# Optimization experiments

Hardware: AMD Instinct MI355X
Metric: run time of the kernel (lower is better)

## Reference

```python
import jax, jax.numpy as jnp
import numpy as np

D, H, KVH, HD = 2048, 16, 8, 128
D1, D2 = 32, 64  # get_decompose_dim(2048)
BITS = 8


def fake_quant(x, bits=BITS):
    # per-row (last-axis) symmetric fake quant with straight-through estimator
    qmax = float(2 ** (bits - 1) - 1)
    s = jnp.maximum(jnp.max(jnp.abs(x), axis=-1, keepdims=True) / qmax, 1e-8)
    q = jnp.clip(jnp.round(x / s), -qmax, qmax) * s
    return x + jax.lax.stop_gradient(q - x)


def rotate_half(x):
    h = x.shape[-1] // 2
    return jnp.concatenate([-x[..., h:], x[..., :h]], axis=-1)


def setup_inputs() -> dict:
    key = jax.random.key(0)
    ks = jax.random.split(key, 10)
    B, S = 1, 2048
    hidden_states = jax.random.normal(ks[0], (B, S, D), jnp.float32)
    # rotary embeddings
    inv_freq = 1.0 / (10000.0 ** (jnp.arange(0, HD, 2, dtype=jnp.float32) / HD))
    t = jnp.arange(S, dtype=jnp.float32)
    freqs = t[:, None] * inv_freq[None, :]
    emb = jnp.concatenate([freqs, freqs], axis=-1)
    cos, sin = jnp.cos(emb)[None], jnp.sin(emb)[None]  # [1,S,HD]
    # projection weights
    Wq = jax.random.normal(ks[1], (H * HD, D), jnp.float32) * 0.02
    Wk = jax.random.normal(ks[2], (KVH * HD, D), jnp.float32) * 0.02
    Wv = jax.random.normal(ks[3], (KVH * HD, D), jnp.float32) * 0.02
    Wo = jax.random.normal(ks[4], (D, H * HD), jnp.float32) * 0.02
    # learned invertible transforms (near-identity for conditioning)
    L = jnp.eye(D1) + 0.02 * jax.random.normal(ks[5], (D1, D1), jnp.float32)
    R = jnp.eye(D2) + 0.02 * jax.random.normal(ks[6], (D2, D2), jnp.float32)
    diag = 1.0 + 0.1 * jax.random.uniform(ks[7], (D,), jnp.float32)
    Tk = jnp.eye(HD) + 0.02 * jax.random.normal(ks[8], (HD, HD), jnp.float32)
    Tv = jnp.eye(HD) + 0.02 * jax.random.normal(ks[9], (HD, HD), jnp.float32)
    return dict(hidden_states=hidden_states, cos=cos, sin=sin, Wq=Wq, Wk=Wk,
                Wv=Wv, Wo=Wo, L=L, R=R, diag=diag, Tk=Tk, Tv=Tv)


def reference(hidden_states, cos, sin, Wq, Wk, Wv, Wo, L, R, diag, Tk, Tv):
    B, S, _ = hidden_states.shape
    groups = H // KVH
    scale = HD ** -0.5
    # ---- ln_trans: x' = (x * diag) @ kron(L, R) ----
    P = diag[:, None] * jnp.kron(L, R)               # [D, D]
    Pinv = jnp.kron(jnp.linalg.inv(L), jnp.linalg.inv(R)) * (1.0 / diag)[None, :]
    x = hidden_states @ P
    x_q = fake_quant(x)                               # per-token activation quant
    # ---- QKV with transform fused into weights (qa_trans), then weight quant ----
    q = x_q @ fake_quant(Wq @ Pinv.T).T               # [B,S,H*HD]
    k = x_q @ fake_quant(Wk @ Pinv.T).T               # [B,S,KVH*HD]
    Wv_eff = jnp.einsum('hd,khD->kdD', Tv, (Wv @ Pinv.T).reshape(KVH, HD, D))
    v = x_q @ fake_quant(Wv_eff.reshape(KVH * HD, D)).T  # v already in Tv space
    # ---- heads + RoPE ----
    q = q.reshape(B, S, H, HD).transpose(0, 2, 1, 3)
    k = k.reshape(B, S, KVH, HD).transpose(0, 2, 1, 3)
    v = v.reshape(B, S, KVH, HD).transpose(0, 2, 1, 3)
    c, s_ = cos[:, None], sin[:, None]                # [1,1,S,HD]
    q = q * c + rotate_half(q) * s_
    k = k * c + rotate_half(k) * s_
    # ---- kcache trans + quant: q @ inv(Tk)^T, k @ Tk (dot product preserved) ----
    q = q @ jnp.linalg.inv(Tk).T
    k = fake_quant(k @ Tk)
    v = fake_quant(v)
    # ---- eager causal attention with GQA ----
    k = jnp.repeat(k, groups, axis=1)
    v = jnp.repeat(v, groups, axis=1)
    scores = jnp.einsum('bhqd,bhkd->bhqk', q, k) * scale
    mask = jnp.tril(jnp.ones((S, S), bool))
    scores = jnp.where(mask, scores, jnp.finfo(scores.dtype).min)
    w = jax.nn.softmax(scores, axis=-1)
    o = jnp.einsum('bhqk,bhkd->bhqd', w, v)
    o = o.transpose(0, 2, 1, 3).reshape(B, S, H * HD)
    # ---- undo vcache trans per head, then quantized o_proj ----
    o = (o.reshape(B, S, H, HD) @ jnp.linalg.inv(Tv)).reshape(B, S, H * HD)
    out = fake_quant(o) @ fake_quant(Wo).T
    return out
```

## Files before the change

kernel.cpp:

```cpp
#include <hip/hip_runtime.h>
#include <math.h>

typedef unsigned short u16;
typedef __attribute__((ext_vector_type(8))) short bf16x8;
typedef __attribute__((ext_vector_type(4))) float f32x4;

__device__ __forceinline__ u16 f2bf(float x) {
    union { float f; unsigned int u; } c; c.f = x;
    unsigned int r = c.u + 0x7fffu + ((c.u >> 16) & 1u);
    return (u16)(r >> 16);
}
__device__ __forceinline__ float bf2f(u16 h) {
    union { unsigned int u; float f; } c; c.u = ((unsigned int)h) << 16;
    return c.f;
}
__device__ __forceinline__ bf16x8 ld16(const u16* p) {
    bf16x8 r;
    ((uint2*)&r)[0] = *(const uint2*)p;
    ((uint2*)&r)[1] = *(const uint2*)(p + 4);
    return r;
}
__device__ __forceinline__ void st8(u16* dst, uint4 r) {
    *(uint2*)dst = make_uint2(r.x, r.y);
    *(uint2*)(dst + 4) = make_uint2(r.z, r.w);
}
__device__ __forceinline__ void cvt8(const float4& v0, const float4& v1,
                                     uint4& hi, uint4& lo) {
    float vv[8] = {v0.x, v0.y, v0.z, v0.w, v1.x, v1.y, v1.z, v1.w};
    u16 h[8], l[8];
#pragma unroll
    for (int e = 0; e < 8; ++e) {
        h[e] = f2bf(vv[e]);
        l[e] = f2bf(vv[e] - bf2f(h[e]));
    }
    hi.x = h[0] | ((unsigned)h[1] << 16); hi.y = h[2] | ((unsigned)h[3] << 16);
    hi.z = h[4] | ((unsigned)h[5] << 16); hi.w = h[6] | ((unsigned)h[7] << 16);
    lo.x = l[0] | ((unsigned)l[1] << 16); lo.y = l[2] | ((unsigned)l[3] << 16);
    lo.z = l[4] | ((unsigned)l[5] << 16); lo.w = l[6] | ((unsigned)l[7] << 16);
}

__global__ __launch_bounds__(1024) void gj4_kernel(
    const float* __restrict__ A0, float* __restrict__ I0,
    const float* __restrict__ A1, float* __restrict__ I1,
    const float* __restrict__ A2, float* __restrict__ I2,
    const float* __restrict__ A3, float* __restrict__ I3) {
    __shared__ float rowbuf[2][128];
    const float* A; float* out; int N;
    switch (blockIdx.x) {
        case 0:  A = A0; out = I0; N = 32;  break;
        case 1:  A = A1; out = I1; N = 64;  break;
        case 2:  A = A2; out = I2; N = 128; break;
        default: A = A3; out = I3; N = 128; break;
    }
    const int tid = threadIdx.x;
    const int i = tid >> 3, g = tid & 7, c0 = g * 16;
    const int rl = (i & 7) << 3;
    float r[16];
#pragma unroll
    for (int e = 0; e < 16; ++e) {
        int j = c0 + e;
        r[e] = (i < N && j < N) ? A[i * N + j] : ((i == j) ? 1.0f : 0.0f);
    }
    if (i == 0) {
        float ip = 1.0f / __shfl(r[0], rl, 64);
#pragma unroll
        for (int e = 0; e < 16; ++e)
            rowbuf[0][c0 + e] = (c0 + e == 0) ? ip : r[e] * ip;
    }
    __syncthreads();
    const int ng = N >> 4;
    for (int k16 = 0; k16 < ng; ++k16) {
#pragma unroll
        for (int e = 0; e < 16; ++e) {
            const int k = (k16 << 4) + e;
            const int pb = k & 1;
            float ci = __shfl(r[e], rl + k16, 64);
            float4 rb0 = *(const float4*)&rowbuf[pb][c0];
            float4 rb1 = *(const float4*)&rowbuf[pb][c0 + 4];
            float4 rb2 = *(const float4*)&rowbuf[pb][c0 + 8];
            float4 rb3 = *(const float4*)&rowbuf[pb][c0 + 12];
            float rb[16] = {rb0.x, rb0.y, rb0.z, rb0.w, rb1.x, rb1.y, rb1.z, rb1.w,
                            rb2.x, rb2.y, rb2.z, rb2.w, rb3.x, rb3.y, rb3.z, rb3.w};
            if (i == k) {
#pragma unroll
                for (int e2 = 0; e2 < 16; ++e2) r[e2] = rb[e2];
            } else {
#pragma unroll
                for (int e2 = 0; e2 < 16; ++e2) {
                    float v = (c0 + e2 == k) ? 0.0f : r[e2];
                    r[e2] = fmaf(-ci, rb[e2], v);
                }
            }
            if (k + 1 < N && i == k + 1) {
                const int en = (e + 1) & 15;
                const int gn = (e == 15) ? k16 + 1 : k16;
                float ip = 1.0f / __shfl(r[en], rl + gn, 64);
#pragma unroll
                for (int e2 = 0; e2 < 16; ++e2)
                    rowbuf[pb ^ 1][c0 + e2] = (c0 + e2 == k + 1) ? ip : r[e2] * ip;
            }
            __syncthreads();
        }
    }
    if (i < N)
#pragma unroll
        for (int e = 0; e < 16; ++e) {
            int j = c0 + e;
            if (j < N) out[i * N + j] = r[e];
        }
}

template <int TA, int TB, int OUTQ, int DIV>
__global__ __launch_bounds__(256) void kron_kernel(
    const float* __restrict__ X, const float* __restrict__ scIn,
    const float* __restrict__ A, const float* __restrict__ B,
    u16* __restrict__ Yq, float* __restrict__ Ysc, float* __restrict__ Yf) {
    __shared__ float Al[32 * 33];
    __shared__ float Bl[64 * 65];
    __shared__ float Xl[32 * 65];
    __shared__ float Tl[32 * 65];
    __shared__ float red[256];
    const int tid = threadIdx.x;
    for (int idx = tid; idx < 1024; idx += 256) {
        int c = idx >> 5, a = idx & 31;
        Al[c * 33 + a] = TA ? A[a * 32 + c] : A[c * 32 + a];
    }
    for (int idx = tid; idx < 4096; idx += 256) {
        int d = idx >> 6, b = idx & 63;
        Bl[d * 65 + b] = TB ? B[b * 64 + d] : B[d * 64 + b];
    }
    const int row = blockIdx.x;
    const float* xp = X + (size_t)row * 2048;
    for (int j = tid; j < 2048; j += 256) {
        float sc = DIV ? (1.0f / scIn[j]) : scIn[j];
        Xl[(j >> 6) * 65 + (j & 63)] = xp[j] * sc;
    }
    __syncthreads();

    const int c = tid >> 3, b0 = (tid & 7) * 8;
    float t[8];
#pragma unroll
    for (int jj = 0; jj < 8; ++jj) t[jj] = 0.0f;
    for (int d = 0; d < 64; ++d) {
        float xv = Xl[c * 65 + d];
#pragma unroll
        for (int jj = 0; jj < 8; ++jj)
            t[jj] = fmaf(xv, Bl[d * 65 + b0 + jj], t[jj]);
    }
#pragma unroll
    for (int jj = 0; jj < 8; ++jj) Tl[c * 65 + b0 + jj] = t[jj];
    __syncthreads();

    const int a = tid >> 3;
    float y[8];
#pragma unroll
    for (int jj = 0; jj < 8; ++jj) y[jj] = 0.0f;
    for (int c2 = 0; c2 < 32; ++c2) {
        float av = Al[c2 * 33 + a];
#pragma unroll
        for (int jj = 0; jj < 8; ++jj)
            y[jj] = fmaf(av, Tl[c2 * 65 + b0 + jj], y[jj]);
    }

    if (OUTQ) {
        float am = 0.0f;
#pragma unroll
        for (int jj = 0; jj < 8; ++jj) am = fmaxf(am, fabsf(y[jj]));
        red[tid] = am;
        __syncthreads();
        for (int s = 128; s > 0; s >>= 1) {
            if (tid < s) red[tid] = fmaxf(red[tid], red[tid + s]);
            __syncthreads();
        }
        float scale = fmaxf(red[0] / 127.0f, 1e-8f);
        if (tid == 0) Ysc[row] = scale;
        u16 qq[8];
#pragma unroll
        for (int e = 0; e < 8; ++e) {
            float v = rintf(y[e] / scale);
            v = fminf(fmaxf(v, -127.0f), 127.0f);
            qq[e] = f2bf(v);
        }
        uint4 pk;
        pk.x = qq[0] | ((unsigned)qq[1] << 16); pk.y = qq[2] | ((unsigned)qq[3] << 16);
        pk.z = qq[4] | ((unsigned)qq[5] << 16); pk.w = qq[6] | ((unsigned)qq[7] << 16);
        *(uint4*)(Yq + (size_t)row * 2048 + tid * 8) = pk;
    } else {
        float* yp = Yf + (size_t)row * 2048 + tid * 8;
        *(float4*)yp = make_float4(y[0], y[1], y[2], y[3]);
        *(float4*)(yp + 4) = make_float4(y[4], y[5], y[6], y[7]);
    }
}

__global__ void split_s_kernel(const float* __restrict__ in, int ld, int cols,
                               u16* __restrict__ hi, u16* __restrict__ lo) {
    int idx = (blockIdx.x * 256 + threadIdx.x) * 4;
    int r = idx / cols, c = idx % cols;
    float4 v = *(const float4*)(in + (size_t)r * ld + c);
    ushort4 h, l;
    h.x = f2bf(v.x); l.x = f2bf(v.x - bf2f(h.x));
    h.y = f2bf(v.y); l.y = f2bf(v.y - bf2f(h.y));
    h.z = f2bf(v.z); l.z = f2bf(v.z - bf2f(h.z));
    h.w = f2bf(v.w); l.w = f2bf(v.w - bf2f(h.w));
    *(ushort4*)(hi + idx) = h;
    *(ushort4*)(lo + idx) = l;
}

__global__ void split_t_kernel(const float* __restrict__ in, u16* __restrict__ hi,
                               u16* __restrict__ lo, int rows, int cols) {
    __shared__ float t[32][33];
    int bx = blockIdx.x, by = blockIdx.y;
    int lx = threadIdx.x & 31, ly = threadIdx.x >> 5;
    for (int r = ly; r < 32; r += 8)
        t[r][lx] = in[(size_t)(by * 32 + r) * cols + bx * 32 + lx];
    __syncthreads();
    for (int r = ly; r < 32; r += 8) {
        float v = t[lx][r];
        size_t o = (size_t)(bx * 32 + r) * rows + by * 32 + lx;
        u16 h = f2bf(v);
        hi[o] = h;
        lo[o] = f2bf(v - bf2f(h));
    }
}

__global__ void split_t3_kernel(const float* __restrict__ i0, u16* __restrict__ h0,
                                u16* __restrict__ l0,
                                const float* __restrict__ i1, u16* __restrict__ h1,
                                u16* __restrict__ l1,
                                const float* __restrict__ i2, u16* __restrict__ h2,
                                u16* __restrict__ l2) {
    __shared__ float t[32][33];
    const float* in; u16* hi; u16* lo;
    switch (blockIdx.z) {
        case 0:  in = i0; hi = h0; lo = l0; break;
        case 1:  in = i1; hi = h1; lo = l1; break;
        default: in = i2; hi = h2; lo = l2; break;
    }
    int bx = blockIdx.x, by = blockIdx.y;
    int lx = threadIdx.x & 31, ly = threadIdx.x >> 5;
    for (int r = ly; r < 32; r += 8)
        t[r][lx] = in[(size_t)(by * 32 + r) * 128 + bx * 32 + lx];
    __syncthreads();
    for (int r = ly; r < 32; r += 8) {
        float v = t[lx][r];
        size_t o = (size_t)(bx * 32 + r) * 128 + by * 32 + lx;
        u16 h = f2bf(v);
        hi[o] = h;
        lo[o] = f2bf(v - bf2f(h));
    }
}

__global__ __launch_bounds__(256) void gemm_kernel(
    const u16* __restrict__ Ah, const u16* __restrict__ Al, int lda, long aZ, int aDiv,
    const u16* __restrict__ Bh, const u16* __restrict__ Bl, int ldb, long bZ, int bDiv,
    float* __restrict__ C, int ldc, long cZ, int cDiv, int K, float alpha) {
    const int m0 = blockIdx.y * 128, n0 = blockIdx.x * 128;
    const int z = blockIdx.z;
    {
        long ao = (long)(z >> aDiv) * aZ;
        long bo = (long)(z >> bDiv) * bZ;
        Ah += ao; Al += ao; Bh += bo; Bl += bo;
    }
    __shared__ u16 Ash[2][2][128][36];
    __shared__ u16 Bsh[2][2][128][36];

    const int tid = threadIdx.x, lane = tid & 63, wave = tid >> 6;
    const int wr = wave >> 1, wc = wave & 1;
    const int fr = lane & 15, fg8 = (lane >> 4) * 8;
    const int srow = tid >> 2, cc8 = (tid & 3) * 8;

    f32x4 acc[4][4];
#pragma unroll
    for (int m = 0; m < 4; ++m)
#pragma unroll
        for (int n = 0; n < 4; ++n) acc[m][n] = (f32x4)0.0f;

    uint4 rah0, rah1, ral0, ral1, rbh0, rbh1, rbl0, rbl1;
    const size_t aoff0 = (size_t)(m0 + srow) * lda + cc8;
    const size_t aoff1 = aoff0 + (size_t)64 * lda;
    const size_t boff0 = (size_t)(n0 + srow) * ldb + cc8;
    const size_t boff1 = boff0 + (size_t)64 * ldb;

#define G_LOAD(k0) { \
    rah0 = *(const uint4*)(Ah + aoff0 + (k0)); rah1 = *(const uint4*)(Ah + aoff1 + (k0)); \
    ral0 = *(const uint4*)(Al + aoff0 + (k0)); ral1 = *(const uint4*)(Al + aoff1 + (k0)); \
    rbh0 = *(const uint4*)(Bh + boff0 + (k0)); rbh1 = *(const uint4*)(Bh + boff1 + (k0)); \
    rbl0 = *(const uint4*)(Bl + boff0 + (k0)); rbl1 = *(const uint4*)(Bl + boff1 + (k0)); }
#define G_STORE(b) { \
    st8(&Ash[b][0][srow][cc8], rah0); st8(&Ash[b][0][srow + 64][cc8], rah1); \
    st8(&Ash[b][1][srow][cc8], ral0); st8(&Ash[b][1][srow + 64][cc8], ral1); \
    st8(&Bsh[b][0][srow][cc8], rbh0); st8(&Bsh[b][0][srow + 64][cc8], rbh1); \
    st8(&Bsh[b][1][srow][cc8], rbl0); st8(&Bsh[b][1][srow + 64][cc8], rbl1); }

    const int nk = K >> 5;
    G_LOAD(0);
    G_STORE(0);
    __syncthreads();
    int cur = 0;
    for (int ik = 0; ik < nk; ++ik) {
        if (ik + 1 < nk) G_LOAD((ik + 1) << 5);
        bf16x8 bh[4], bl[4];
#pragma unroll
        for (int n = 0; n < 4; ++n) {
            bh[n] = ld16(&Bsh[cur][0][wc * 64 + n * 16 + fr][fg8]);
            bl[n] = ld16(&Bsh[cur][1][wc * 64 + n * 16 + fr][fg8]);
        }
#pragma unroll
        for (int m = 0; m < 4; ++m) {
            bf16x8 ah = ld16(&Ash[cur][0][wr * 64 + m * 16 + fr][fg8]);
            bf16x8 al = ld16(&Ash[cur][1][wr * 64 + m * 16 + fr][fg8]);
#pragma unroll
            for (int n = 0; n < 4; ++n) {
                acc[m][n] = __builtin_amdgcn_mfma_f32_16x16x32_bf16(ah, bh[n], acc[m][n], 0, 0, 0);
                acc[m][n] = __builtin_amdgcn_mfma_f32_16x16x32_bf16(ah, bl[n], acc[m][n], 0, 0, 0);
                acc[m][n] = __builtin_amdgcn_mfma_f32_16x16x32_bf16(al, bh[n], acc[m][n], 0, 0, 0);
            }
        }
        if (ik + 1 < nk) G_STORE(cur ^ 1);
        __syncthreads();
        cur ^= 1;
    }
    const long co = (long)(z >> cDiv) * cZ;
#pragma unroll
    for (int m = 0; m < 4; ++m) {
        int row_b = m0 + wr * 64 + m * 16 + (fg8 >> 1);
#pragma unroll
        for (int n = 0; n < 4; ++n) {
            int col = n0 + wc * 64 + n * 16 + fr;
#pragma unroll
            for (int j = 0; j < 4; ++j)
                C[co + (long)(row_b + j) * ldc + col] = alpha * acc[m][n][j];
        }
    }
#undef G_LOAD
#undef G_STORE
}

__global__ __launch_bounds__(256) void gemm_af32_kernel(
    const float* __restrict__ A, int lda, long aZ, int aDiv,
    const u16* __restrict__ Bh, const u16* __restrict__ Bl, int ldb, long bZ, int bDiv,
    float* __restrict__ C, int ldc, long cZ, int cDiv, int K, float alpha) {
    const int m0 = blockIdx.y * 128, n0 = blockIdx.x * 128;
    const int z = blockIdx.z;
    A += (long)(z >> aDiv) * aZ;
    {
        long bo = (long)(z >> bDiv) * bZ;
        Bh += bo; Bl += bo;
    }
    __shared__ u16 Ash[2][2][128][36];
    __shared__ u16 Bsh[2][2][128][36];

    const int tid = threadIdx.x, lane = tid & 63, wave = tid >> 6;
    const int wr = wave >> 1, wc = wave & 1;
    const int fr = lane & 15, fg8 = (lane >> 4) * 8;
    const int srow = tid >> 2, cc8 = (tid & 3) * 8;

    f32x4 acc[4][4];
#pragma unroll
    for (int m = 0; m < 4; ++m)
#pragma unroll
        for (int n = 0; n < 4; ++n) acc[m][n] = (f32x4)0.0f;

    float4 a00, a01, a10, a11;
    uint4 rbh0, rbh1, rbl0, rbl1;
    const size_t aoff0 = (size_t)(m0 + srow) * lda + cc8;
    const size_t aoff1 = aoff0 + (size_t)64 * lda;
    const size_t boff0 = (size_t)(n0 + srow) * ldb + cc8;
    const size_t boff1 = boff0 + (size_t)64 * ldb;

#define GA_LOAD(k0) { \
    a00 = *(const float4*)(A + aoff0 + (k0)); a01 = *(const float4*)(A + aoff0 + (k0) + 4); \
    a10 = *(const float4*)(A + aoff1 + (k0)); a11 = *(const float4*)(A + aoff1 + (k0) + 4); \
    rbh0 = *(const uint4*)(Bh + boff0 + (k0)); rbh1 = *(const uint4*)(Bh + boff1 + (k0)); \
    rbl0 = *(const uint4*)(Bl + boff0 + (k0)); rbl1 = *(const uint4*)(Bl + boff1 + (k0)); }
#define GA_STORE(b) { \
    uint4 h0_, l0_, h1_, l1_; \
    cvt8(a00, a01, h0_, l0_); cvt8(a10, a11, h1_, l1_); \
    st8(&Ash[b][0][srow][cc8], h0_); st8(&Ash[b][0][srow + 64][cc8], h1_); \
    st8(&Ash[b][1][srow][cc8], l0_); st8(&Ash[b][1][srow + 64][cc8], l1_); \
    st8(&Bsh[b][0][srow][cc8], rbh0); st8(&Bsh[b][0][srow + 64][cc8], rbh1); \
    st8(&Bsh[b][1][srow][cc8], rbl0); st8(&Bsh[b][1][srow + 64][cc8], rbl1); }

    const int nk = K >> 5;
    GA_LOAD(0);
    GA_STORE(0);
    __syncthreads();
    int cur = 0;
    for (int ik = 0; ik < nk; ++ik) {
        if (ik + 1 < nk) GA_LOAD((ik + 1) << 5);
        bf16x8 bh[4], bl[4];
#pragma unroll
        for (int n = 0; n < 4; ++n) {
            bh[n] = ld16(&Bsh[cur][0][wc * 64 + n * 16 + fr][fg8]);
            bl[n] = ld16(&Bsh[cur][1][wc * 64 + n * 16 + fr][fg8]);
        }
#pragma unroll
        for (int m = 0; m < 4; ++m) {
            bf16x8 ah = ld16(&Ash[cur][0][wr * 64 + m * 16 + fr][fg8]);
            bf16x8 al = ld16(&Ash[cur][1][wr * 64 + m * 16 + fr][fg8]);
#pragma unroll
            for (int n = 0; n < 4; ++n) {
                acc[m][n] = __builtin_amdgcn_mfma_f32_16x16x32_bf16(ah, bh[n], acc[m][n], 0, 0, 0);
                acc[m][n] = __builtin_amdgcn_mfma_f32_16x16x32_bf16(ah, bl[n], acc[m][n], 0, 0, 0);
                acc[m][n] = __builtin_amdgcn_mfma_f32_16x16x32_bf16(al, bh[n], acc[m][n], 0, 0, 0);
            }
        }
        if (ik + 1 < nk) GA_STORE(cur ^ 1);
        __syncthreads();
        cur ^= 1;
    }
    const long co = (long)(z >> cDiv) * cZ;
#pragma unroll
    for (int m = 0; m < 4; ++m) {
        int row_b = m0 + wr * 64 + m * 16 + (fg8 >> 1);
#pragma unroll
        for (int n = 0; n < 4; ++n) {
            int col = n0 + wc * 64 + n * 16 + fr;
#pragma unroll
            for (int j = 0; j < 4; ++j)
                C[co + (long)(row_b + j) * ldc + col] = alpha * acc[m][n][j];
        }
    }
#undef GA_LOAD
#undef GA_STORE
}

__global__ __launch_bounds__(256) void gemm_int_kernel(
    const u16* __restrict__ A, int lda, const float* __restrict__ sa,
    const u16* __restrict__ B, int ldb, const float* __restrict__ sb,
    float* __restrict__ C, int ldc, long aZ, long bZ, long cZ, int K) {
    const int m0 = blockIdx.y * 128, n0 = blockIdx.x * 128;
    const int z = blockIdx.z;
    A += (long)z * aZ; B += (long)z * bZ; C += (long)z * cZ;
    __shared__ u16 Ash[2][128][36];
    __shared__ u16 Bsh[2][128][36];
    const int tid = threadIdx.x, lane = tid & 63, wave = tid >> 6;
    const int wr = wave >> 1, wc = wave & 1;
    const int fr = lane & 15, fg8 = (lane >> 4) * 8;
    const int srow = tid >> 2, cc8 = (tid & 3) * 8;
    f32x4 acc[4][4];
#pragma unroll
    for (int m = 0; m < 4; ++m)
#pragma unroll
        for (int n = 0; n < 4; ++n) acc[m][n] = (f32x4)0.0f;

    uint4 ra0, ra1, rb0, rb1;
    const size_t aoff0 = (size_t)(m0 + srow) * lda + cc8;
    const size_t aoff1 = aoff0 + (size_t)64 * lda;
    const size_t boff0 = (size_t)(n0 + srow) * ldb + cc8;
    const size_t boff1 = boff0 + (size_t)64 * ldb;
#define GI_LOAD(k0) { \
    ra0 = *(const uint4*)(A + aoff0 + (k0)); ra1 = *(const uint4*)(A + aoff1 + (k0)); \
    rb0 = *(const uint4*)(B + boff0 + (k0)); rb1 = *(const uint4*)(B + boff1 + (k0)); }
#define GI_STORE(b) { \
    st8(&Ash[b][srow][cc8], ra0); st8(&Ash[b][srow + 64][cc8], ra1); \
    st8(&Bsh[b][srow][cc8], rb0); st8(&Bsh[b][srow + 64][cc8], rb1); }
    const int nk = K >> 5;
    GI_LOAD(0);
    GI_STORE(0);
    __syncthreads();
    int cur = 0;
    for (int ik = 0; ik < nk; ++ik) {
        if (ik + 1 < nk) GI_LOAD((ik + 1) << 5);
        bf16x8 bfr[4];
#pragma unroll
        for (int n = 0; n < 4; ++n)
            bfr[n] = ld16(&Bsh[cur][wc * 64 + n * 16 + fr][fg8]);
#pragma unroll
        for (int m = 0; m < 4; ++m) {
            bf16x8 ah = ld16(&Ash[cur][wr * 64 + m * 16 + fr][fg8]);
#pragma unroll
            for (int n = 0; n < 4; ++n)
                acc[m][n] = __builtin_amdgcn_mfma_f32_16x16x32_bf16(ah, bfr[n], acc[m][n], 0, 0, 0);
        }
        if (ik + 1 < nk) GI_STORE(cur ^ 1);
        __syncthreads();
        cur ^= 1;
    }
#pragma unroll
    for (int m = 0; m < 4; ++m) {
        int row_b = m0 + wr * 64 + m * 16 + (fg8 >> 1);
#pragma unroll
        for (int n = 0; n < 4; ++n) {
            int col = n0 + wc * 64 + n * 16 + fr;
            float sc = sb[col];
#pragma unroll
            for (int j = 0; j < 4; ++j)
                C[(long)(row_b + j) * ldc + col] = acc[m][n][j] * sa[row_b + j] * sc;
        }
    }
#undef GI_LOAD
#undef GI_STORE
}

__global__ void rowquant_int_kernel(const float* __restrict__ x, u16* __restrict__ qi,
                                    float* __restrict__ sc, int cols) {
    __shared__ float red[256];
    int row = blockIdx.x, tid = threadIdx.x;
    const float* p = x + (size_t)row * cols;
    u16* q = qi + (size_t)row * cols;
    float m = 0.0f;
    for (int j = tid; j < cols; j += 256) m = fmaxf(m, fabsf(p[j]));
    red[tid] = m; __syncthreads();
    for (int s = 128; s > 0; s >>= 1) {
        if (tid < s) red[tid] = fmaxf(red[tid], red[tid + s]);
        __syncthreads();
    }
    float scale = fmaxf(red[0] / 127.0f, 1e-8f);
    if (tid == 0) sc[row] = scale;
    for (int j = tid; j < cols; j += 256) {
        float v = rintf(p[j] / scale);
        v = fminf(fmaxf(v, -127.0f), 127.0f);
        q[j] = f2bf(v);
    }
}

__global__ void rowquant_w_kernel(const float* __restrict__ x, u16* __restrict__ qi,
                                  float* __restrict__ sc) {
    int row = blockIdx.x * 4 + (threadIdx.x >> 6);
    int lane = threadIdx.x & 63;
    const float* p = x + (size_t)row * 128;
    float2 v = *(const float2*)(p + lane * 2);
    float m = fmaxf(fabsf(v.x), fabsf(v.y));
#pragma unroll
    for (int off = 1; off < 64; off <<= 1) m = fmaxf(m, __shfl_xor(m, off));
    float scale = fmaxf(m / 127.0f, 1e-8f);
    if (lane == 0) sc[row] = scale;
    float a = rintf(v.x / scale), b = rintf(v.y / scale);
    a = fminf(fmaxf(a, -127.0f), 127.0f);
    b = fminf(fmaxf(b, -127.0f), 127.0f);
    unsigned pk = f2bf(a) | ((unsigned)f2bf(b) << 16);
    *(unsigned*)(qi + (size_t)row * 128 + lane * 2) = pk;
}

__global__ __launch_bounds__(256) void quantT_v_kernel(
    const float* __restrict__ QKVf, u16* __restrict__ vTi, float* __restrict__ vs) {
    __shared__ u16 tile[128][72];
    const int st = blockIdx.x, g = blockIdx.y;
    const int t = threadIdx.x;
    const int sl = t >> 2, dc = (t & 3) * 32;
    const int s = st * 64 + sl;
    const float* p = QKVf + (size_t)s * 4096 + 3072 + g * 128 + dc;
    float4 vr[8];
    float m = 0.0f;
#pragma unroll
    for (int q = 0; q < 8; ++q) {
        vr[q] = *(const float4*)(p + q * 4);
        m = fmaxf(m, fmaxf(fmaxf(fabsf(vr[q].x), fabsf(vr[q].y)),
                           fmaxf(fabsf(vr[q].z), fabsf(vr[q].w))));
    }
    m = fmaxf(m, __shfl_xor(m, 1));
    m = fmaxf(m, __shfl_xor(m, 2));
    float scale = fmaxf(m / 127.0f, 1e-8f);
    if ((t & 3) == 0) vs[s * 8 + g] = scale;
#pragma unroll
    for (int q = 0; q < 8; ++q) {
        float vv[4] = {vr[q].x, vr[q].y, vr[q].z, vr[q].w};
#pragma unroll
        for (int e = 0; e < 4; ++e) {
            float qv = rintf(vv[e] / scale);
            qv = fminf(fmaxf(qv, -127.0f), 127.0f);
            tile[dc + q * 4 + e][sl] = f2bf(qv);
        }
    }
    __syncthreads();
    const int d = t >> 1, sc0 = (t & 1) * 32;
    u16* dst = vTi + (size_t)(g * 128 + d) * 2048 + st * 64 + sc0;
#pragma unroll
    for (int q = 0; q < 4; ++q) {
        u16 tmp[8];
#pragma unroll
        for (int e = 0; e < 8; ++e) tmp[e] = tile[d][sc0 + q * 8 + e];
        uint4 v;
        v.x = tmp[0] | ((unsigned)tmp[1] << 16); v.y = tmp[2] | ((unsigned)tmp[3] << 16);
        v.z = tmp[4] | ((unsigned)tmp[5] << 16); v.w = tmp[6] | ((unsigned)tmp[7] << 16);
        *(uint4*)(dst + q * 8) = v;
    }
}

__global__ void rope_kernel(float* __restrict__ x, int ld, int cb,
                            const float* __restrict__ c, const float* __restrict__ s,
                            int nh) {
    int idx = blockIdx.x * 256 + threadIdx.x;
    int d = idx & 63;
    int t = idx >> 6;
    int h = t % nh;
    int sq = t / nh;
    size_t base = (size_t)sq * ld + cb + h * 128;
    float a = x[base + d], b = x[base + d + 64];
    float c1 = c[sq * 128 + d], s1 = s[sq * 128 + d];
    float c2 = c[sq * 128 + d + 64], s2 = s[sq * 128 + d + 64];
    x[base + d] = a * c1 - b * s1;
    x[base + d + 64] = b * c2 + a * s2;
}

__global__ __launch_bounds__(256, 2) void flash_kernel(
    const float* __restrict__ q2f,
    const u16* __restrict__ k2i, const float* __restrict__ ksc,
    const u16* __restrict__ vTi, const float* __restrict__ vsc,
    float* __restrict__ obuf, float* __restrict__ mlbuf) {
    const int h = blockIdx.x, part = blockIdx.y, qt = 31 - blockIdx.z, g = h >> 1;
    __shared__ u16 Ksh[2][64 * 128];
    __shared__ u16 Vsh[2][128 * 64];
    __shared__ u16 Psh[4][16 * 64];
    __shared__ float Kss[2][64];
    __shared__ float Vss[2][64];

    const int tid = threadIdx.x, lane = tid & 63, w = tid >> 6;
    const int lc = lane & 15, lg = lane >> 4;
    const float scale = 0.08838834764831845f;
    const float LOG2E = 1.4426950408889634f;
    const float THR = 10.0f;

    bf16x8 qh[4], ql[4];
    {
        int s = qt * 64 + w * 16 + lc;
        const float* qp = q2f + (size_t)s * 2048 + h * 128 + lg * 8;
#pragma unroll
        for (int kk = 0; kk < 4; ++kk) {
            float4 v0 = *(const float4*)(qp + kk * 32);
            float4 v1 = *(const float4*)(qp + kk * 32 + 4);
            float vv[8] = {v0.x, v0.y, v0.z, v0.w, v1.x, v1.y, v1.z, v1.w};
#pragma unroll
            for (int e = 0; e < 8; ++e) {
                float x = vv[e] * scale;
                u16 hh = f2bf(x);
                qh[kk][e] = (short)hh;
                ql[kk][e] = (short)f2bf(x - bf2f(hh));
            }
        }
    }

    f32x4 acc_o[8];
#pragma unroll
    for (int nn = 0; nn < 8; ++nn) acc_o[nn] = (f32x4)0.0f;
    float mj = -1e30f, lj = 0.0f;

    const int p0cnt = (qt + 2) >> 1;
    const int tn = (part == 0) ? p0cnt : (qt + 1 - p0cnt);
    const int t0 = (part == 0) ? 0 : p0cnt;

    const int kr = tid >> 2, kc = tid & 3;
    const int vd = tid >> 1, vc0 = (tid & 1) * 4;
    uint4 kg0, kg1, kg2, kg3, vg0, vg1, vg2, vg3;
    float sreg = 0.0f;

#define STAGE_LOAD(tg) { \
    const int j0_ = (tg) * 64; \
    const u16* kp_ = k2i + (size_t)(j0_ + kr) * 1024 + g * 128; \
    kg0 = *(const uint4*)(kp_ + kc * 8); \
    kg1 = *(const uint4*)(kp_ + (kc + 4) * 8); \
    kg2 = *(const uint4*)(kp_ + (kc + 8) * 8); \
    kg3 = *(const uint4*)(kp_ + (kc + 12) * 8); \
    const u16* vp_ = vTi + (size_t)(g * 128 + vd) * 2048 + j0_; \
    vg0 = *(const uint4*)(vp_ + vc0 * 8); \
    vg1 = *(const uint4*)(vp_ + (vc0 + 1) * 8); \
    vg2 = *(const uint4*)(vp_ + (vc0 + 2) * 8); \
    vg3 = *(const uint4*)(vp_ + (vc0 + 3) * 8); \
    if (tid < 64) sreg = ksc[(j0_ + tid) * 8 + g] * LOG2E; \
    else if (tid < 128) sreg = vsc[(j0_ + tid - 64) * 8 + g]; }

#define STAGE_WRITE(b) { \
    *(uint4*)(&Ksh[b][kr * 128 + ((kc ^ (kr & 7)) << 3)]) = kg0; \
    *(uint4*)(&Ksh[b][kr * 128 + (((kc + 4) ^ (kr & 7)) << 3)]) = kg1; \
    *(uint4*)(&Ksh[b][kr * 128 + (((kc + 8) ^ (kr & 7)) << 3)]) = kg2; \
    *(uint4*)(&Ksh[b][kr * 128 + (((kc + 12) ^ (kr & 7)) << 3)]) = kg3; \
    *(uint4*)(&Vsh[b][vd * 64 + ((vc0 ^ (vd & 7)) << 3)]) = vg0; \
    *(uint4*)(&Vsh[b][vd * 64 + (((vc0 + 1) ^ (vd & 7)) << 3)]) = vg1; \
    *(uint4*)(&Vsh[b][vd * 64 + (((vc0 + 2) ^ (vd & 7)) << 3)]) = vg2; \
    *(uint4*)(&Vsh[b][vd * 64 + (((vc0 + 3) ^ (vd & 7)) << 3)]) = vg3; \
    if (tid < 64) Kss[b][tid] = sreg; \
    else if (tid < 128) Vss[b][tid - 64] = sreg; }

    if (tn > 0) {
        STAGE_LOAD(t0);
        STAGE_WRITE(0);
    }
    __syncthreads();
    for (int t = 0; t < tn; ++t) {
        const int cur = t & 1;
        const int tg = t0 + t;
        if (t + 1 < tn) STAGE_LOAD(t0 + t + 1);

        f32x4 accs[4];
#pragma unroll
        for (int n = 0; n < 4; ++n) accs[n] = (f32x4)0.0f;
#pragma unroll
        for (int n = 0; n < 4; ++n) {
#pragma unroll
            for (int kk = 0; kk < 4; ++kk) {
                bf16x8 kf = ld16(&Ksh[cur][(n * 16 + lc) * 128 + (((kk * 4 + lg) ^ (lc & 7)) << 3)]);
                accs[n] = __builtin_amdgcn_mfma_f32_16x16x32_bf16(kf, qh[kk], accs[n], 0, 0, 0);
                accs[n] = __builtin_amdgcn_mfma_f32_16x16x32_bf16(kf, ql[kk], accs[n], 0, 0, 0);
            }
        }
#pragma unroll
        for (int n = 0; n < 4; ++n)
#pragma unroll
            for (int j = 0; j < 4; ++j)
                accs[n][j] *= Kss[cur][n * 16 + lg * 4 + j];
        if (tg == qt) {
            int qg = qt * 64 + w * 16 + lc;
#pragma unroll
            for (int n = 0; n < 4; ++n)
#pragma unroll
                for (int j = 0; j < 4; ++j) {
                    int kgl = tg * 64 + n * 16 + lg * 4 + j;
                    if (kgl > qg) accs[n][j] = -3.0e38f;
                }
        }

        float pm = accs[0][0];
#pragma unroll
        for (int n = 0; n < 4; ++n)
#pragma unroll
            for (int j = 0; j < 4; ++j) pm = fmaxf(pm, accs[n][j]);
        pm = fmaxf(pm, __shfl_xor(pm, 16));
        pm = fmaxf(pm, __shfl_xor(pm, 32));
        bool need = pm > mj + THR;
        float mn = need ? pm : mj;
        float sf = need ? exp2f(mj - mn) : 1.0f;
        mj = mn;
        if (__any(need)) {
            float sfj[4];
#pragma unroll
            for (int j = 0; j < 4; ++j) sfj[j] = __shfl(sf, lg * 4 + j);
#pragma unroll
            for (int nn = 0; nn < 8; ++nn)
#pragma unroll
                for (int j = 0; j < 4; ++j) acc_o[nn][j] *= sfj[j];
        }
        float rowsum = 0.0f;
#pragma unroll
        for (int n = 0; n < 4; ++n)
#pragma unroll
            for (int j = 0; j < 4; ++j) {
                float p = exp2f(accs[n][j] - mj);
                accs[n][j] = p;
                rowsum += p;
            }
        rowsum += __shfl_xor(rowsum, 16);
        rowsum += __shfl_xor(rowsum, 32);
        lj = lj * sf + rowsum;

#pragma unroll
        for (int n = 0; n < 4; ++n)
#pragma unroll
            for (int jp = 0; jp < 2; ++jp) {
                int k = n * 16 + lg * 4 + jp * 2;
                unsigned val = f2bf(accs[n][jp * 2] * Vss[cur][k]) |
                               ((unsigned)f2bf(accs[n][jp * 2 + 1] * Vss[cur][k + 1]) << 16);
                int cch = k >> 3;
                *(unsigned*)(&Psh[w][lc * 64 + ((cch ^ (lc & 7)) << 3) + (k & 7)]) = val;
            }
        bf16x8 pf[2];
#pragma unroll
        for (int kk = 0; kk < 2; ++kk)
            pf[kk] = ld16(&Psh[w][lc * 64 + (((kk * 4 + lg) ^ (lc & 7)) << 3)]);

#pragma unroll
        for (int nn = 0; nn < 8; ++nn) {
            int d = nn * 16 + lc;
#pragma unroll
            for (int kk = 0; kk < 2; ++kk) {
                bf16x8 vf = ld16(&Vsh[cur][d * 64 + (((kk * 4 + lg) ^ (d & 7)) << 3)]);
                acc_o[nn] = __builtin_amdgcn_mfma_f32_16x16x32_bf16(pf[kk], vf, acc_o[nn], 0, 0, 0);
            }
        }
        if (t + 1 < tn) STAGE_WRITE(cur ^ 1);
        __syncthreads();
    }
#undef STAGE_LOAD
#undef STAGE_WRITE

    float* op = obuf + (size_t)part * 4194304 + ((size_t)h * 2048 + qt * 64 + w * 16) * 128;
#pragma unroll
    for (int nn = 0; nn < 8; ++nn)
#pragma unroll
        for (int j = 0; j < 4; ++j)
            op[(lg * 4 + j) * 128 + nn * 16 + lc] = acc_o[nn][j];
    if (lg == 0) {
        int rs = h * 2048 + qt * 64 + w * 16 + lc;
        mlbuf[part * 65536 + rs] = mj;
        mlbuf[part * 65536 + 32768 + rs] = lj;
    }
}

__global__ void combine_kernel(const float* __restrict__ o01,
                               const float* __restrict__ ml,
                               float* __restrict__ of) {
    int idx = blockIdx.x * 256 + threadIdx.x;
    int hs = idx >> 7;
    float m0 = ml[hs], l0 = ml[32768 + hs];
    float m1 = ml[65536 + hs], l1 = ml[98304 + hs];
    float m = fmaxf(m0, m1);
    float w0 = exp2f(m0 - m), w1 = exp2f(m1 - m);
    float l = l0 * w0 + l1 * w1;
    of[idx] = (o01[idx] * w0 + o01[4194304 + idx] * w1) / l;
}

__global__ void add2_kernel(const float* __restrict__ a, const float* __restrict__ b,
                            float* __restrict__ o) {
    int i = (blockIdx.x * 256 + threadIdx.x) * 4;
    float4 x = *(const float4*)(a + i);
    float4 y = *(const float4*)(b + i);
    x.x += y.x; x.y += y.y; x.z += y.z; x.w += y.w;
    *(float4*)(o + i) = x;
}

extern "C" void kernel_launch(void* const* d_in, const int* in_sizes, int n_in,
                              void* d_out, int out_size, void* d_ws, size_t ws_size,
                              hipStream_t stream) {
    const float* hidden = (const float*)d_in[0];
    const float* cosp   = (const float*)d_in[1];
    const float* sinp   = (const float*)d_in[2];
    const float* Wq     = (const float*)d_in[3];
    const float* Wk     = (const float*)d_in[4];
    const float* Wv     = (const float*)d_in[5];
    const float* Wo     = (const float*)d_in[6];
    const float* Lp     = (const float*)d_in[7];
    const float* Rp     = (const float*)d_in[8];
    const float* diag   = (const float*)d_in[9];
    const float* Tkp    = (const float*)d_in[10];
    const float* Tvp    = (const float*)d_in[11];
    float* out = (float*)d_out;

    const size_t MiB = 1ull << 20;
    char* W = (char*)d_ws;
    auto F = [&](size_t mb) { return (float*)(W + mb * MiB); };
    auto U = [&](size_t mb) { return (u16*)(W + mb * MiB); };
    const long HP2 = 2097152;

    float* dsc   = (float*)d_out;
    float* invL  = dsc;
    float* invR  = dsc + 1024;
    float* invTk = dsc + 5120;
    float* invTv = dsc + 21504;
    u16* sm = (u16*)(dsc + 37888);
    u16* invTk_sh = sm;              u16* invTk_sl = sm + 16384;
    u16* TkT_sh   = sm + 2 * 16384;  u16* TkT_sl   = sm + 3 * 16384;
    u16* invTvT_sh= sm + 4 * 16384;  u16* invTvT_sl= sm + 5 * 16384;
    u16* TvT_sh   = sm + 6 * 16384;  u16* TvT_sl   = sm + 7 * 16384;

    float* xs    = F(88);
    float* wqkvs = xs + 2048;
    float* wqs   = wqkvs;
    float* wks   = wqkvs + 2048;
    float* wvs   = wqkvs + 3072;
    float* k2s   = wqkvs + 4096;
    float* vs    = k2s + 16384;
    float* o2s   = vs + 16384;
    float* wos   = o2s + 2048;

    gj4_kernel<<<4, 1024, 0, stream>>>(Lp, invL, Rp, invR, Tkp, invTk, Tvp, invTv);
    split_s_kernel<<<16, 256, 0, stream>>>(invTk, 128, 128, invTk_sh, invTk_sl);
    split_t3_kernel<<<dim3(4, 4, 3), 256, 0, stream>>>(
        Tkp, TkT_sh, TkT_sl, invTv, invTvT_sh, invTvT_sl, Tvp, TvT_sh, TvT_sl);

    u16* Xi    = U(0);
    u16* WQKVi = U(8);
    u16* WVi   = U(20);
    float* WvP = F(24);
    kron_kernel<0, 0, 1, 0><<<2048, 256, 0, stream>>>(hidden, diag, Lp, Rp, Xi, xs, 0);
    kron_kernel<1, 1, 1, 1><<<2048, 256, 0, stream>>>(Wq, diag, invL, invR, WQKVi, wqs, 0);
    kron_kernel<1, 1, 1, 1><<<1024, 256, 0, stream>>>(Wk, diag, invL, invR, U(16), wks, 0);
    kron_kernel<1, 1, 0, 1><<<1024, 256, 0, stream>>>(Wv, diag, invL, invR, 0, 0, WvP);

    u16* WVPt_s = U(32);
    split_t_kernel<<<dim3(64, 32), 256, 0, stream>>>(WvP, WVPt_s, WVPt_s + HP2, 1024, 2048);
    float* WVf = F(72);
    gemm_kernel<<<dim3(16, 1, 8), 256, 0, stream>>>(
        TvT_sh, TvT_sl, 128, 0, 0, WVPt_s, WVPt_s + HP2, 1024, 128, 0,
        WVf, 2048, (long)128 * 2048, 0, 128, 1.0f);
    rowquant_int_kernel<<<1024, 256, 0, stream>>>(WVf, WVi, wvs, 2048);

    float* QKVf = F(40);
    gemm_int_kernel<<<dim3(32, 16), 256, 0, stream>>>(Xi, 2048, xs, WQKVi, 2048, wqkvs,
                                                      QKVf, 4096, 0, 0, 0, 2048);

    rope_kernel<<<8192, 256, 0, stream>>>(QKVf, 4096, 0, cosp, sinp, 16);
    rope_kernel<<<4096, 256, 0, stream>>>(QKVf, 4096, 2048, cosp, sinp, 8);

    float* k2f = F(32);
    gemm_af32_kernel<<<dim3(1, 16, 8), 256, 0, stream>>>(
        QKVf + 2048, 4096, 128, 0, TkT_sh, TkT_sl, 128, 0, 0,
        k2f, 1024, 128, 0, 128, 1.0f);
    u16* k2i = U(8);
    rowquant_w_kernel<<<4096, 256, 0, stream>>>(k2f, k2i, k2s);

    u16* vTi = U(16);
    quantT_v_kernel<<<dim3(32, 8), 256, 0, stream>>>(QKVf, vTi, vs);

    float* q2f = F(72);
    gemm_af32_kernel<<<dim3(1, 16, 16), 256, 0, stream>>>(
        QKVf, 4096, 128, 0, invTk_sh, invTk_sl, 128, 0, 0,
        q2f, 2048, 128, 0, 128, 1.0f);

    float* o01 = F(40);
    float* ml  = F(32);
    flash_kernel<<<dim3(16, 2, 32), 256, 0, stream>>>(q2f, k2i, k2s, vTi, vs, o01, ml);
    float* of = F(0);
    combine_kernel<<<16384, 256, 0, stream>>>(o01, ml, of);

    float* o2f = F(16);
    gemm_af32_kernel<<<dim3(1, 16, 16), 256, 0, stream>>>(
        of, 128, 262144, 0, invTvT_sh, invTvT_sl, 128, 0, 0,
        o2f, 2048, 128, 0, 128, 1.0f);
    u16* o2i = U(32);
    rowquant_int_kernel<<<2048, 256, 0, stream>>>(o2f, o2i, o2s, 2048);
    u16* Woi = U(40);
    rowquant_int_kernel<<<2048, 256, 0, stream>>>(Wo, Woi, wos, 2048);
    float* C0 = F(48);
    gemm_int_kernel<<<dim3(16, 16, 2), 256, 0, stream>>>(o2i, 2048, o2s, Woi, 2048, wos,
                                                         C0, 2048, 1024, 1024, 4194304, 1024);
    add2_kernel<<<4096, 256, 0, stream>>>(C0, C0 + 4194304, out);

    (void)in_sizes; (void)n_in; (void)out_size; (void)ws_size;
}
```

Measured before the change: 497.7 us.

## Replace per-column Gauss-Jordan inversion with 16-wide blocked elimination

The small-matrix inverse kernel now does blocked Gauss-Jordan in 16-column panels. One wave inverts the 16x16 pivot block with shuffles, and the whole block applies a rank-16 update from shared memory. This cuts the block-wide barriers from one per column (up to 128) to four per panel, so eight panels. In exchange, the pivot-block inversion is serialized on 16 threads and each panel does more shared-memory traffic. It also always runs eight panels even for the smaller N=32 and N=64 matrices, which are padded with identity.

```diff
diff --git a/kernel.cpp b/kernel.cpp
--- a/kernel.cpp
+++ b/kernel.cpp
@@ -44,7 +44,10 @@
     const float* __restrict__ A1, float* __restrict__ I1,
     const float* __restrict__ A2, float* __restrict__ I2,
     const float* __restrict__ A3, float* __restrict__ I3) {
-    __shared__ float rowbuf[2][128];
+    __shared__ float Cc[128][17];
+    __shared__ float Ur[16][132];
+    __shared__ float Pn[16][132];
+    __shared__ float El[16][17];
     const float* A; float* out; int N;
     switch (blockIdx.x) {
         case 0:  A = A0; out = I0; N = 32;  break;
@@ -53,54 +56,81 @@
         default: A = A3; out = I3; N = 128; break;
     }
     const int tid = threadIdx.x;
-    const int i = tid >> 3, g = tid & 7, c0 = g * 16;
-    const int rl = (i & 7) << 3;
+    const int i = tid >> 3, seg = tid & 7, c0 = seg * 16;
     float r[16];
 #pragma unroll
     for (int e = 0; e < 16; ++e) {
         int j = c0 + e;
         r[e] = (i < N && j < N) ? A[i * N + j] : ((i == j) ? 1.0f : 0.0f);
     }
-    if (i == 0) {
-        float ip = 1.0f / __shfl(r[0], rl, 64);
-#pragma unroll
-        for (int e = 0; e < 16; ++e)
-            rowbuf[0][c0 + e] = (c0 + e == 0) ? ip : r[e] * ip;
-    }
-    __syncthreads();
-    const int ng = N >> 4;
-    for (int k16 = 0; k16 < ng; ++k16) {
-#pragma unroll
-        for (int e = 0; e < 16; ++e) {
-            const int k = (k16 << 4) + e;
-            const int pb = k & 1;
-            float ci = __shfl(r[e], rl + k16, 64);
-            float4 rb0 = *(const float4*)&rowbuf[pb][c0];
-            float4 rb1 = *(const float4*)&rowbuf[pb][c0 + 4];
-            float4 rb2 = *(const float4*)&rowbuf[pb][c0 + 8];
-            float4 rb3 = *(const float4*)&rowbuf[pb][c0 + 12];
-            float rb[16] = {rb0.x, rb0.y, rb0.z, rb0.w, rb1.x, rb1.y, rb1.z, rb1.w,
-                            rb2.x, rb2.y, rb2.z, rb2.w, rb3.x, rb3.y, rb3.z, rb3.w};
-            if (i == k) {
-#pragma unroll
-                for (int e2 = 0; e2 < 16; ++e2) r[e2] = rb[e2];
+    for (int s = 0; s < 8; ++s) {
+        if (seg == s) {
+#pragma unroll
+            for (int e = 0; e < 16; ++e) Cc[i][e] = r[e];
+        }
+        if ((i >> 4) == s) {
+#pragma unroll
+            for (int e = 0; e < 16; ++e) Ur[i & 15][c0 + e] = r[e];
+        }
+        __syncthreads();
+        if (tid < 16) {
+            float d[16];
+#pragma unroll
+            for (int m = 0; m < 16; ++m) d[m] = Cc[s * 16 + tid][m];
+#pragma unroll
+            for (int k = 0; k < 16; ++k) {
+                float piv = 1.0f / __shfl(d[k], k);
+                if (tid == k) {
+#pragma unroll
+                    for (int j = 0; j < 16; ++j) d[j] = (j == k) ? piv : d[j] * piv;
+                }
+                float f = d[k];
+#pragma unroll
+                for (int j = 0; j < 16; ++j) {
+                    if (j != k) {
+                        float rkj = __shfl(d[j], k);
+                        if (tid != k) d[j] = fmaf(-f, rkj, d[j]);
+                    }
+                }
+                if (tid != k) d[k] = -f * piv;
+            }
+#pragma unroll
+            for (int m = 0; m < 16; ++m) El[tid][m] = d[m];
+        }
+        __syncthreads();
+#pragma unroll
+        for (int o = 0; o < 2; ++o) {
+            int idx = tid * 2 + o;
+            int m = idx >> 7, j = idx & 127;
+            float acc;
+            if ((j >> 4) == s) {
+                acc = El[m][j & 15];
             } else {
-#pragma unroll
-                for (int e2 = 0; e2 < 16; ++e2) {
-                    float v = (c0 + e2 == k) ? 0.0f : r[e2];
-                    r[e2] = fmaf(-ci, rb[e2], v);
-                }
+                acc = 0.0f;
+#pragma unroll
+                for (int t = 0; t < 16; ++t)
+                    acc = fmaf(El[m][t], Ur[t][j], acc);
             }
-            if (k + 1 < N && i == k + 1) {
-                const int en = (e + 1) & 15;
-                const int gn = (e == 15) ? k16 + 1 : k16;
-                float ip = 1.0f / __shfl(r[en], rl + gn, 64);
-#pragma unroll
-                for (int e2 = 0; e2 < 16; ++e2)
-                    rowbuf[pb ^ 1][c0 + e2] = (c0 + e2 == k + 1) ? ip : r[e2] * ip;
+            Pn[m][j] = acc;
+        }
+        __syncthreads();
+        float C_[16];
+#pragma unroll
+        for (int m = 0; m < 16; ++m) C_[m] = Cc[i][m];
+        if ((i >> 4) == s) {
+#pragma unroll
+            for (int e = 0; e < 16; ++e) r[e] = Pn[i & 15][c0 + e];
+        } else {
+#pragma unroll
+            for (int e = 0; e < 16; ++e) {
+                float v = (seg == s) ? 0.0f : r[e];
+#pragma unroll
+                for (int m = 0; m < 16; ++m)
+                    v = fmaf(-C_[m], Pn[m][c0 + e], v);
+                r[e] = v;
             }
-            __syncthreads();
-        }
+        }
+        __syncthreads();
     }
     if (i < N)
 #pragma unroll
```

Measured after the change: 524.3 us. 5.3% more time.

## Merge matrix inversion and activation Kronecker transform into one launch

Applied to the files above, without the earlier changes.

Combines the 4-block Gauss-Jordan inversion kernel with the hidden-state Kronecker transform and quantization into a single 2052-block launch. The 2048 extra blocks process activation rows with 1024 threads each while the four inversion blocks run alongside them. This removes the serial, poorly parallel inversion stage from the critical path and saves one launch. In exchange, the activation rows now run with 1024-thread blocks and a larger shared reduction buffer, which may lower occupancy compared with the former 256-thread kron kernel.

```diff
diff --git a/kernel.cpp b/kernel.cpp
--- a/kernel.cpp
+++ b/kernel.cpp
@@ -39,75 +39,143 @@
     lo.z = l[4] | ((unsigned)l[5] << 16); lo.w = l[6] | ((unsigned)l[7] << 16);
 }
 
-__global__ __launch_bounds__(1024) void gj4_kernel(
+__global__ __launch_bounds__(1024) void p0_kernel(
     const float* __restrict__ A0, float* __restrict__ I0,
     const float* __restrict__ A1, float* __restrict__ I1,
     const float* __restrict__ A2, float* __restrict__ I2,
-    const float* __restrict__ A3, float* __restrict__ I3) {
-    __shared__ float rowbuf[2][128];
-    const float* A; float* out; int N;
-    switch (blockIdx.x) {
-        case 0:  A = A0; out = I0; N = 32;  break;
-        case 1:  A = A1; out = I1; N = 64;  break;
-        case 2:  A = A2; out = I2; N = 128; break;
-        default: A = A3; out = I3; N = 128; break;
-    }
+    const float* __restrict__ A3, float* __restrict__ I3,
+    const float* __restrict__ X, const float* __restrict__ dg,
+    const float* __restrict__ Lk, const float* __restrict__ Rk,
+    u16* __restrict__ Yq, float* __restrict__ Ysc) {
     const int tid = threadIdx.x;
-    const int i = tid >> 3, g = tid & 7, c0 = g * 16;
-    const int rl = (i & 7) << 3;
-    float r[16];
-#pragma unroll
-    for (int e = 0; e < 16; ++e) {
-        int j = c0 + e;
-        r[e] = (i < N && j < N) ? A[i * N + j] : ((i == j) ? 1.0f : 0.0f);
-    }
-    if (i == 0) {
-        float ip = 1.0f / __shfl(r[0], rl, 64);
-#pragma unroll
-        for (int e = 0; e < 16; ++e)
-            rowbuf[0][c0 + e] = (c0 + e == 0) ? ip : r[e] * ip;
-    }
-    __syncthreads();
-    const int ng = N >> 4;
-    for (int k16 = 0; k16 < ng; ++k16) {
-#pragma unroll
-        for (int e = 0; e < 16; ++e) {
-            const int k = (k16 << 4) + e;
-            const int pb = k & 1;
-            float ci = __shfl(r[e], rl + k16, 64);
-            float4 rb0 = *(const float4*)&rowbuf[pb][c0];
-            float4 rb1 = *(const float4*)&rowbuf[pb][c0 + 4];
-            float4 rb2 = *(const float4*)&rowbuf[pb][c0 + 8];
-            float4 rb3 = *(const float4*)&rowbuf[pb][c0 + 12];
-            float rb[16] = {rb0.x, rb0.y, rb0.z, rb0.w, rb1.x, rb1.y, rb1.z, rb1.w,
-                            rb2.x, rb2.y, rb2.z, rb2.w, rb3.x, rb3.y, rb3.z, rb3.w};
-            if (i == k) {
-#pragma unroll
-                for (int e2 = 0; e2 < 16; ++e2) r[e2] = rb[e2];
-            } else {
-#pragma unroll
-                for (int e2 = 0; e2 < 16; ++e2) {
-                    float v = (c0 + e2 == k) ? 0.0f : r[e2];
-                    r[e2] = fmaf(-ci, rb[e2], v);
-                }
-            }
-            if (k + 1 < N && i == k + 1) {
-                const int en = (e + 1) & 15;
-                const int gn = (e == 15) ? k16 + 1 : k16;
-                float ip = 1.0f / __shfl(r[en], rl + gn, 64);
-#pragma unroll
-                for (int e2 = 0; e2 < 16; ++e2)
-                    rowbuf[pb ^ 1][c0 + e2] = (c0 + e2 == k + 1) ? ip : r[e2] * ip;
-            }
-            __syncthreads();
-        }
-    }
-    if (i < N)
+    if (blockIdx.x < 4) {
+        __shared__ float rowbuf[2][128];
+        const float* A; float* out; int N;
+        switch (blockIdx.x) {
+            case 0:  A = A0; out = I0; N = 32;  break;
+            case 1:  A = A1; out = I1; N = 64;  break;
+            case 2:  A = A2; out = I2; N = 128; break;
+            default: A = A3; out = I3; N = 128; break;
+        }
+        const int i = tid >> 3, g = tid & 7, c0 = g * 16;
+        const int rl = (i & 7) << 3;
+        float r[16];
 #pragma unroll
         for (int e = 0; e < 16; ++e) {
             int j = c0 + e;
-            if (j < N) out[i * N + j] = r[e];
-        }
+            r[e] = (i < N && j < N) ? A[i * N + j] : ((i == j) ? 1.0f : 0.0f);
+        }
+        if (i == 0) {
+            float ip = 1.0f / __shfl(r[0], rl, 64);
+#pragma unroll
+            for (int e = 0; e < 16; ++e)
+                rowbuf[0][c0 + e] = (c0 + e == 0) ? ip : r[e] * ip;
+        }
+        __syncthreads();
+        const int ng = N >> 4;
+        for (int k16 = 0; k16 < ng; ++k16) {
+#pragma unroll
+            for (int e = 0; e < 16; ++e) {
+                const int k = (k16 << 4) + e;
+                const int pb = k & 1;
+                float ci = __shfl(r[e], rl + k16, 64);
+                float4 rb0 = *(const float4*)&rowbuf[pb][c0];
+                float4 rb1 = *(const float4*)&rowbuf[pb][c0 + 4];
+                float4 rb2 = *(const float4*)&rowbuf[pb][c0 + 8];
+                float4 rb3 = *(const float4*)&rowbuf[pb][c0 + 12];
+                float rb[16] = {rb0.x, rb0.y, rb0.z, rb0.w, rb1.x, rb1.y, rb1.z, rb1.w,
+                                rb2.x, rb2.y, rb2.z, rb2.w, rb3.x, rb3.y, rb3.z, rb3.w};
+                if (i == k) {
+#pragma unroll
+                    for (int e2 = 0; e2 < 16; ++e2) r[e2] = rb[e2];
+                } else {
+#pragma unroll
+                    for (int e2 = 0; e2 < 16; ++e2) {
+                        float v = (c0 + e2 == k) ? 0.0f : r[e2];
+                        r[e2] = fmaf(-ci, rb[e2], v);
+                    }
+                }
+                if (k + 1 < N && i == k + 1) {
+                    const int en = (e + 1) & 15;
+                    const int gn = (e == 15) ? k16 + 1 : k16;
+                    float ip = 1.0f / __shfl(r[en], rl + gn, 64);
+#pragma unroll
+                    for (int e2 = 0; e2 < 16; ++e2)
+                        rowbuf[pb ^ 1][c0 + e2] = (c0 + e2 == k + 1) ? ip : r[e2] * ip;
+                }
+                __syncthreads();
+            }
+        }
+        if (i < N)
+#pragma unroll
+            for (int e = 0; e < 16; ++e) {
+                int j = c0 + e;
+                if (j < N) out[i * N + j] = r[e];
+            }
+    } else {
+        __shared__ float Al[32 * 33];
+        __shared__ float Bl[64 * 65];
+        __shared__ float Xl[32 * 65];
+        __shared__ float Tl[32 * 65];
+        __shared__ float red[1024];
+        if (tid < 1024) {
+            int c = tid >> 5, a = tid & 31;
+            Al[c * 33 + a] = Lk[c * 32 + a];
+        }
+        for (int idx = tid; idx < 4096; idx += 1024) {
+            int d = idx >> 6, b = idx & 63;
+            Bl[d * 65 + b] = Rk[d * 64 + b];
+        }
+        const int row = blockIdx.x - 4;
+        const float* xp = X + (size_t)row * 2048;
+        for (int j = tid; j < 2048; j += 1024)
+            Xl[(j >> 6) * 65 + (j & 63)] = xp[j] * dg[j];
+        __syncthreads();
+
+        float t2[2], y2[2];
+#pragma unroll
+        for (int o = 0; o < 2; ++o) {
+            int idx = tid * 2 + o;
+            int c = idx >> 6, b = idx & 63;
+            float acc = 0.0f;
+            for (int d = 0; d < 64; ++d)
+                acc = fmaf(Xl[c * 65 + d], Bl[d * 65 + b], acc);
+            t2[o] = acc;
+        }
+        {
+            int idx0 = tid * 2;
+            Tl[(idx0 >> 6) * 65 + (idx0 & 63)] = t2[0];
+            Tl[((idx0 + 1) >> 6) * 65 + ((idx0 + 1) & 63)] = t2[1];
+        }
+        __syncthreads();
+#pragma unroll
+        for (int o = 0; o < 2; ++o) {
+            int idx = tid * 2 + o;
+            int a = idx >> 6, b = idx & 63;
+            float acc = 0.0f;
+            for (int c2 = 0; c2 < 32; ++c2)
+                acc = fmaf(Al[c2 * 33 + a], Tl[c2 * 65 + b], acc);
+            y2[o] = acc;
+        }
+        float am = fmaxf(fabsf(y2[0]), fabsf(y2[1]));
+        red[tid] = am;
+        __syncthreads();
+        for (int s = 512; s > 0; s >>= 1) {
+            if (tid < s) red[tid] = fmaxf(red[tid], red[tid + s]);
+            __syncthreads();
+        }
+        float scale = fmaxf(red[0] / 127.0f, 1e-8f);
+        if (tid == 0) Ysc[row] = scale;
+        unsigned pk;
+        {
+            float v0 = rintf(y2[0] / scale);
+            v0 = fminf(fmaxf(v0, -127.0f), 127.0f);
+            float v1 = rintf(y2[1] / scale);
+            v1 = fminf(fmaxf(v1, -127.0f), 127.0f);
+            pk = f2bf(v0) | ((unsigned)f2bf(v1) << 16);
+        }
+        *(unsigned*)(Yq + (size_t)row * 2048 + tid * 2) = pk;
+    }
 }
 
 template <int TA, int TB, int OUTQ, int DIV>
@@ -852,16 +920,16 @@
     float* o2s   = vs + 16384;
     float* wos   = o2s + 2048;
 
-    gj4_kernel<<<4, 1024, 0, stream>>>(Lp, invL, Rp, invR, Tkp, invTk, Tvp, invTv);
+    u16* Xi = U(0);
+    p0_kernel<<<2052, 1024, 0, stream>>>(Lp, invL, Rp, invR, Tkp, invTk, Tvp, invTv,
+                                         hidden, diag, Lp, Rp, Xi, xs);
     split_s_kernel<<<16, 256, 0, stream>>>(invTk, 128, 128, invTk_sh, invTk_sl);
     split_t3_kernel<<<dim3(4, 4, 3), 256, 0, stream>>>(
         Tkp, TkT_sh, TkT_sl, invTv, invTvT_sh, invTvT_sl, Tvp, TvT_sh, TvT_sl);
 
-    u16* Xi    = U(0);
     u16* WQKVi = U(8);
     u16* WVi   = U(20);
     float* WvP = F(24);
-    kron_kernel<0, 0, 1, 0><<<2048, 256, 0, stream>>>(hidden, diag, Lp, Rp, Xi, xs, 0);
     kron_kernel<1, 1, 1, 1><<<2048, 256, 0, stream>>>(Wq, diag, invL, invR, WQKVi, wqs, 0);
     kron_kernel<1, 1, 1, 1><<<1024, 256, 0, stream>>>(Wk, diag, invL, invR, U(16), wks, 0);
     kron_kernel<1, 1, 0, 1><<<1024, 256, 0, stream>>>(Wv, diag, invL, invR, 0, 0, WvP);
```

After: 459.5 us. 1.08x faster.
